# Performance work log

Measured on AMD Instinct MI355X. Metric: run time of the kernel, lower is better.

Reference implementation:

```python
import jax, jax.numpy as jnp
import numpy as np

K = 3  # hardcoded in TransitionUp.forward

def setup_inputs() -> dict:
    key = jax.random.key(0)
    ks = jax.random.split(key, 8)
    M, N = 32768, 8192
    UP_C, DOWN_C, OUT_C = 128, 256, 128
    return {
        "up_points": jax.random.normal(ks[0], (M, 3), dtype=jnp.float32),
        "up_features": jax.random.normal(ks[1], (M, UP_C), dtype=jnp.float32),
        "down_points": jax.random.normal(ks[2], (N, 3), dtype=jnp.float32),
        "down_features": jax.random.normal(ks[3], (N, DOWN_C), dtype=jnp.float32),
        # torch nn.Linear params: W [out,in], b [out]
        "W_up": jax.random.normal(ks[4], (OUT_C, UP_C), dtype=jnp.float32) / np.sqrt(UP_C),
        "b_up": jax.random.normal(ks[5], (OUT_C,), dtype=jnp.float32) * 0.01,
        "W_down": jax.random.normal(ks[6], (OUT_C, DOWN_C), dtype=jnp.float32) / np.sqrt(DOWN_C),
        "b_down": jax.random.normal(ks[7], (OUT_C,), dtype=jnp.float32) * 0.01,
    }

def interpolate_knn(query_points, dataset_points, dataset_features, k):
    # squared pairwise distances [M, N]
    delta = query_points[:, None, :] - dataset_points[None, :, :]
    dist = jnp.sum(delta * delta, axis=-1)
    neg_dist, knn_idx = jax.lax.top_k(-dist, k)  # smallest-k
    knn_dist = -neg_dist                           # [M, k]
    knn_feats = dataset_features[knn_idx]          # [M, k, C]
    recip = 1.0 / (knn_dist + 1e-8)
    weights = recip / jnp.sum(recip, axis=-1, keepdims=True)  # [M, k]
    return jnp.einsum('mk,mkc->mc', weights, knn_feats)

def reference(up_points, up_features, down_points, down_features, W_up, b_up, W_down, b_down):
    down_f = down_features @ W_down.T + b_down            # [N, OUT_C]
    interp_f = interpolate_knn(up_points, down_points, down_f, K)  # [M, OUT_C]
    return interp_f + (up_features @ W_up.T + b_up)
```

## Files before the change

kernel.cpp:

```cpp
#include <hip/hip_runtime.h>
#include <cfloat>

#define M_UP   32768
#define N_DOWN 8192
#define UPC    128
#define DOWNC  256
#define OUTC   128
#define NCHUNK 8
#define CHUNK  (N_DOWN / NCHUNK)
#define G      8
#define Q      2
#define PG     12

__device__ __forceinline__ void fma4(float4& acc, float s, const float4 w) {
    acc.x = fmaf(s, w.x, acc.x);
    acc.y = fmaf(s, w.y, acc.y);
    acc.z = fmaf(s, w.z, acc.z);
    acc.w = fmaf(s, w.w, acc.w);
}

__device__ __forceinline__ void top3_bl(float s, int idx,
                                        float& d0, float& d1, float& d2,
                                        int& i0, int& i1, int& i2) {
    bool c0 = s < d0, c1 = s < d1, c2 = s < d2;
    float n0 = fminf(d0, s);
    float n1 = __builtin_amdgcn_fmed3f(d0, d1, s);
    float n2 = __builtin_amdgcn_fmed3f(d1, d2, s);
    int m0 = c0 ? idx : i0;
    int m1 = c0 ? i0 : (c1 ? idx : i1);
    int m2 = c1 ? i1 : (c2 ? idx : i2);
    d0 = n0; d1 = n1; d2 = n2;
    i0 = m0; i1 = m1; i2 = m2;
}

__global__ __launch_bounds__(256) void transpose_w(
        const float* __restrict__ W_up, const float* __restrict__ W_down,
        float* __restrict__ wt_up, float* __restrict__ wt_down) {
    int e = blockIdx.x * 256 + threadIdx.x;
    if (e < DOWNC * OUTC) {
        int k = e >> 7, c = e & 127;
        wt_down[e] = W_down[c * DOWNC + k];
    } else {
        int e2 = e - DOWNC * OUTC;
        int k = e2 >> 7, c = e2 & 127;
        wt_up[e2] = W_up[c * UPC + k];
    }
}

template <int K>
__device__ __forceinline__ void gemm_tile32(
        const float* __restrict__ A, const float* __restrict__ WT,
        float* sA , float* sW ,
        int rbase, int tid, float4 acc[2][2]) {
    const int rl = tid & 15;
    const int c0 = (tid >> 4) * 8;
    #pragma unroll 1
    for (int ph = 0; ph < K / 32; ++ph) {
        if (ph) __syncthreads();
        {
            int r = tid >> 3, k4 = tid & 7;
            float4 v = *(const float4*)(A + (size_t)(rbase + r) * K + ph * 32 + k4 * 4);
            *(float4*)&sA[r * 36 + k4 * 4] = v;
        }
        #pragma unroll
        for (int i = 0; i < 4; ++i) {
            int idx = tid + i * 256;
            int kk = idx >> 5, cc = idx & 31;
            float4 v = *(const float4*)(WT + (size_t)(ph * 32 + kk) * OUTC + cc * 4);
            *(float4*)&sW[kk * OUTC + cc * 4] = v;
        }
        __syncthreads();
        #pragma unroll 4
        for (int kk = 0; kk < 32; ++kk) {
            float a0 = sA[rl * 36 + kk];
            float a1 = sA[(rl + 16) * 36 + kk];
            float4 w0 = *(const float4*)&sW[kk * OUTC + c0];
            float4 w1 = *(const float4*)&sW[kk * OUTC + c0 + 4];
            fma4(acc[0][0], a0, w0); fma4(acc[0][1], a0, w1);
            fma4(acc[1][0], a1, w0); fma4(acc[1][1], a1, w1);
        }
    }
}

__device__ __forceinline__ void down_body(
        const float* __restrict__ A, const float* __restrict__ WT,
        const float* __restrict__ bias, float* __restrict__ down_f,
        int rb, int tid, float* smem) {
    float* sA = smem;
    float* sW = smem + 1152;
    float4 acc[2][2] = {};
    gemm_tile32<DOWNC>(A, WT, sA, sW, rb * 32, tid, acc);
    const int rl = tid & 15;
    const int cg = (tid >> 4) * 2;
    const float4 b0 = ((const float4*)bias)[cg];
    const float4 b1 = ((const float4*)bias)[cg + 1];
    #pragma unroll
    for (int i = 0; i < 2; ++i) {
        const int row = rb * 32 + rl + 16 * i;
        float4 v0 = acc[i][0], v1 = acc[i][1];
        v0.x += b0.x; v0.y += b0.y; v0.z += b0.z; v0.w += b0.w;
        v1.x += b1.x; v1.y += b1.y; v1.z += b1.z; v1.w += b1.w;
        ((float4*)down_f)[row * 32 + cg] = v0;
        ((float4*)down_f)[row * 32 + cg + 1] = v1;
    }
}

__device__ __forceinline__ void knn_body(
        const float* __restrict__ up_points,
        const float* __restrict__ down_points,
        float2* __restrict__ part,
        int bx, int by, int tid, float* smem) {
    float* sx = smem;
    float* sy = smem + 1536;
    float* sz = smem + 3072;
    const int base = by * CHUNK;
    for (int t = tid; t < CHUNK; t += 256) {
        int g = base + t;
        int gi = t >> 3, j = t & 7;
        sx[PG * gi + j] = down_points[3 * g];
        sy[PG * gi + j] = down_points[3 * g + 1];
        sz[PG * gi + j] = down_points[3 * g + 2];
    }
    __syncthreads();

    const int m0 = bx * (256 * Q) + tid;
    const int m1 = m0 + 256;
    const float q0x = up_points[3 * m0];
    const float q0y = up_points[3 * m0 + 1];
    const float q0z = up_points[3 * m0 + 2];
    const float q1x = up_points[3 * m1];
    const float q1y = up_points[3 * m1 + 1];
    const float q1z = up_points[3 * m1 + 2];

    float a_gd0 = FLT_MAX, a_gd1 = FLT_MAX, a_gd2 = FLT_MAX;
    int   a_gi0 = 0, a_gi1 = 0, a_gi2 = 0;
    float b_gd0 = FLT_MAX, b_gd1 = FLT_MAX, b_gd2 = FLT_MAX;
    int   b_gi0 = 0, b_gi1 = 0, b_gi2 = 0;

    for (int gi = 0; gi < CHUNK / G; ++gi) {
        float4 x0 = *(const float4*)&sx[PG * gi], x1 = *(const float4*)&sx[PG * gi + 4];
        float4 y0 = *(const float4*)&sy[PG * gi], y1 = *(const float4*)&sy[PG * gi + 4];
        float4 z0 = *(const float4*)&sz[PG * gi], z1 = *(const float4*)&sz[PG * gi + 4];
        float px[G] = {x0.x, x0.y, x0.z, x0.w, x1.x, x1.y, x1.z, x1.w};
        float py[G] = {y0.x, y0.y, y0.z, y0.w, y1.x, y1.y, y1.z, y1.w};
        float pz[G] = {z0.x, z0.y, z0.z, z0.w, z1.x, z1.y, z1.z, z1.w};
        float s0[G], s1[G];
        #pragma unroll
        for (int j = 0; j < G; ++j) {
            float dx0 = q0x - px[j], dy0 = q0y - py[j], dz0 = q0z - pz[j];
            s0[j] = fmaf(dz0, dz0, fmaf(dy0, dy0, dx0 * dx0));
            float dx1 = q1x - px[j], dy1 = q1y - py[j], dz1 = q1z - pz[j];
            s1[j] = fmaf(dz1, dz1, fmaf(dy1, dy1, dx1 * dx1));
        }
        float gm0 = fminf(fminf(fminf(s0[0], s0[1]), fminf(s0[2], s0[3])),
                          fminf(fminf(s0[4], s0[5]), fminf(s0[6], s0[7])));
        float gm1 = fminf(fminf(fminf(s1[0], s1[1]), fminf(s1[2], s1[3])),
                          fminf(fminf(s1[4], s1[5]), fminf(s1[6], s1[7])));
        top3_bl(gm0, gi, a_gd0, a_gd1, a_gd2, a_gi0, a_gi1, a_gi2);
        top3_bl(gm1, gi, b_gd0, b_gd1, b_gd2, b_gi0, b_gi1, b_gi2);
    }

    #pragma unroll
    for (int qq = 0; qq < Q; ++qq) {
        const float qx = qq ? q1x : q0x;
        const float qy = qq ? q1y : q0y;
        const float qz = qq ? q1z : q0z;
        int bases[3];
        if (qq == 0) { bases[0] = a_gi0; bases[1] = a_gi1; bases[2] = a_gi2; }
        else         { bases[0] = b_gi0; bases[1] = b_gi1; bases[2] = b_gi2; }
        float D0 = FLT_MAX, D1 = FLT_MAX, D2 = FLT_MAX;
        int I0 = 0, I1 = 0, I2 = 0;
        #pragma unroll
        for (int t = 0; t < 3; ++t) {
            const int gb = bases[t];
            float4 x0 = *(const float4*)&sx[PG * gb], x1 = *(const float4*)&sx[PG * gb + 4];
            float4 y0 = *(const float4*)&sy[PG * gb], y1 = *(const float4*)&sy[PG * gb + 4];
            float4 z0 = *(const float4*)&sz[PG * gb], z1 = *(const float4*)&sz[PG * gb + 4];
            float px[G] = {x0.x, x0.y, x0.z, x0.w, x1.x, x1.y, x1.z, x1.w};
            float py[G] = {y0.x, y0.y, y0.z, y0.w, y1.x, y1.y, y1.z, y1.w};
            float pz[G] = {z0.x, z0.y, z0.z, z0.w, z1.x, z1.y, z1.z, z1.w};
            #pragma unroll
            for (int j = 0; j < G; ++j) {
                float dx = qx - px[j], dy = qy - py[j], dz = qz - pz[j];
                float s = fmaf(dz, dz, fmaf(dy, dy, dx * dx));
                top3_bl(s, base + gb * G + j, D0, D1, D2, I0, I1, I2);
            }
        }
        const int m = qq ? m1 : m0;
        const int o = (by * M_UP + m) * 3;
        part[o]     = make_float2(D0, __int_as_float(I0));
        part[o + 1] = make_float2(D1, __int_as_float(I1));
        part[o + 2] = make_float2(D2, __int_as_float(I2));
    }
}

__global__ __launch_bounds__(256) void fused_dp_knn(
        const float* __restrict__ down_features, const float* __restrict__ wt_down,
        const float* __restrict__ b_down, float* __restrict__ down_f,
        const float* __restrict__ up_points, const float* __restrict__ down_points,
        float2* __restrict__ part) {
    __shared__ __align__(16) float smem[5248];
    const int bid = blockIdx.x;
    if (bid < 512) {
        knn_body(up_points, down_points, part, bid & 63, bid >> 6,
                 threadIdx.x, smem);
    } else {
        down_body(down_features, wt_down, b_down, down_f, bid - 512,
                  threadIdx.x, smem);
    }
}

__global__ __launch_bounds__(256) void up_fused(
        const float* __restrict__ A, const float* __restrict__ WT,
        const float* __restrict__ bias, const float* __restrict__ down_f,
        const float2* __restrict__ part,
        float* __restrict__ out) {
    __shared__ __align__(16) float sAT[32][72];
    __shared__ __align__(16) float sW[32][128];
    const int tid = threadIdx.x;
    const int rt4 = (tid >> 4) * 4;
    const int ct  = tid & 15;
    const int rbase = blockIdx.x * 64;

    float4 acc[4][2] = {};
    #pragma unroll 1
    for (int ph = 0; ph < UPC / 32; ++ph) {
        if (ph) __syncthreads();
        {
            const int r = tid & 63, kq = tid >> 6;
            const float* Ar = A + (size_t)(rbase + r) * UPC + ph * 32 + kq * 8;
            float4 v0 = *(const float4*)Ar;
            float4 v1 = *(const float4*)(Ar + 4);
            const int k0 = kq * 8;
            sAT[k0 + 0][r] = v0.x; sAT[k0 + 1][r] = v0.y;
            sAT[k0 + 2][r] = v0.z; sAT[k0 + 3][r] = v0.w;
            sAT[k0 + 4][r] = v1.x; sAT[k0 + 5][r] = v1.y;
            sAT[k0 + 6][r] = v1.z; sAT[k0 + 7][r] = v1.w;
        }
        {
            const float4* Wp = (const float4*)(WT + (size_t)ph * 32 * OUTC);
            float4* sW4 = (float4*)&sW[0][0];
            #pragma unroll
            for (int i = 0; i < 4; ++i)
                sW4[tid + i * 256] = Wp[tid + i * 256];
        }
        __syncthreads();
        #pragma unroll 4
        for (int kk = 0; kk < 32; ++kk) {
            float4 a  = *(const float4*)&sAT[kk][rt4];
            float4 w0 = *(const float4*)&sW[kk][ct * 4];
            float4 w1 = *(const float4*)&sW[kk][64 + ct * 4];
            fma4(acc[0][0], a.x, w0); fma4(acc[0][1], a.x, w1);
            fma4(acc[1][0], a.y, w0); fma4(acc[1][1], a.y, w1);
            fma4(acc[2][0], a.z, w0); fma4(acc[2][1], a.z, w1);
            fma4(acc[3][0], a.w, w0); fma4(acc[3][1], a.w, w1);
        }
    }

    const float4 b0 = ((const float4*)bias)[ct];
    const float4 b1 = ((const float4*)bias)[ct + 16];
    const float4* df4 = (const float4*)down_f;
    float4* out4 = (float4*)out;
    #pragma unroll
    for (int i = 0; i < 4; ++i) {
        const int m = rbase + rt4 + i;
        float D0 = FLT_MAX, D1 = FLT_MAX, D2 = FLT_MAX;
        int I0 = 0, I1 = 0, I2 = 0;
        #pragma unroll
        for (int s = 0; s < NCHUNK; ++s) {
            const float2* p = part + ((size_t)s * M_UP + m) * 3;
            float2 v0 = p[0], v1 = p[1], v2 = p[2];
            top3_bl(v0.x, __float_as_int(v0.y), D0, D1, D2, I0, I1, I2);
            top3_bl(v1.x, __float_as_int(v1.y), D0, D1, D2, I0, I1, I2);
            top3_bl(v2.x, __float_as_int(v2.y), D0, D1, D2, I0, I1, I2);
        }
        float r0 = 1.f / (D0 + 1e-8f);
        float r1 = 1.f / (D1 + 1e-8f);
        float r2 = 1.f / (D2 + 1e-8f);
        float rs = (r0 + r1) + r2;
        float w0 = r0 / rs, w1 = r1 / rs, w2 = r2 / rs;
        float4 f00 = df4[I0 * 32 + ct], f01 = df4[I0 * 32 + ct + 16];
        float4 f10 = df4[I1 * 32 + ct], f11 = df4[I1 * 32 + ct + 16];
        float4 f20 = df4[I2 * 32 + ct], f21 = df4[I2 * 32 + ct + 16];
        float4 res0, res1;
        res0.x = acc[i][0].x + b0.x + fmaf(w0, f00.x, fmaf(w1, f10.x, w2 * f20.x));
        res0.y = acc[i][0].y + b0.y + fmaf(w0, f00.y, fmaf(w1, f10.y, w2 * f20.y));
        res0.z = acc[i][0].z + b0.z + fmaf(w0, f00.z, fmaf(w1, f10.z, w2 * f20.z));
        res0.w = acc[i][0].w + b0.w + fmaf(w0, f00.w, fmaf(w1, f10.w, w2 * f20.w));
        res1.x = acc[i][1].x + b1.x + fmaf(w0, f01.x, fmaf(w1, f11.x, w2 * f21.x));
        res1.y = acc[i][1].y + b1.y + fmaf(w0, f01.y, fmaf(w1, f11.y, w2 * f21.y));
        res1.z = acc[i][1].z + b1.z + fmaf(w0, f01.z, fmaf(w1, f11.z, w2 * f21.z));
        res1.w = acc[i][1].w + b1.w + fmaf(w0, f01.w, fmaf(w1, f11.w, w2 * f21.w));
        out4[m * 32 + ct] = res0;
        out4[m * 32 + ct + 16] = res1;
    }
}

extern "C" void kernel_launch(void* const* d_in, const int* in_sizes, int n_in,
                              void* d_out, int out_size, void* d_ws, size_t ws_size,
                              hipStream_t stream) {
    const float* up_points     = (const float*)d_in[0];
    const float* up_features   = (const float*)d_in[1];
    const float* down_points   = (const float*)d_in[2];
    const float* down_features = (const float*)d_in[3];
    const float* W_up          = (const float*)d_in[4];
    const float* b_up          = (const float*)d_in[5];
    const float* W_down        = (const float*)d_in[6];
    const float* b_down        = (const float*)d_in[7];
    float* out = (float*)d_out;

    float* wt_down = (float*)d_ws;
    float* wt_up   = wt_down + DOWNC * OUTC;
    float* down_f  = wt_up + UPC * OUTC;
    float2* part   = (float2*)(down_f + N_DOWN * OUTC);

    transpose_w<<<(DOWNC * OUTC + UPC * OUTC) / 256, 256, 0, stream>>>(
        W_up, W_down, wt_up, wt_down);
    fused_dp_knn<<<768, 256, 0, stream>>>(
        down_features, wt_down, b_down, down_f, up_points, down_points, part);
    up_fused<<<M_UP / 64, 256, 0, stream>>>(
        up_features, wt_up, b_up, down_f, part, out);
}
```

Before: 167.9 us.

## Move up-projection GEMM into fused kNN kernel and add separate merge pass

The up_features GEMM now runs as extra block roles inside the fused kNN/down-projection kernel, with block IDs interleaved 2 kNN : 1 down : 2 up per group of 5, so its work can overlap the compute-heavy kNN blocks. A new lightweight merge kernel stages the partial top-3 lists in shared memory, merges them, gathers down_f rows, and adds the interpolation into out with a read-modify-write. This trades an extra round trip of the output tensor through global memory and a larger shared allocation for better load balance across the GPU.

```diff
diff --git a/kernel.cpp b/kernel.cpp
--- a/kernel.cpp
+++ b/kernel.cpp
@@ -194,33 +194,15 @@
     }
 }
 
-__global__ __launch_bounds__(256) void fused_dp_knn(
-        const float* __restrict__ down_features, const float* __restrict__ wt_down,
-        const float* __restrict__ b_down, float* __restrict__ down_f,
-        const float* __restrict__ up_points, const float* __restrict__ down_points,
-        float2* __restrict__ part) {
-    __shared__ __align__(16) float smem[5248];
-    const int bid = blockIdx.x;
-    if (bid < 512) {
-        knn_body(up_points, down_points, part, bid & 63, bid >> 6,
-                 threadIdx.x, smem);
-    } else {
-        down_body(down_features, wt_down, b_down, down_f, bid - 512,
-                  threadIdx.x, smem);
-    }
-}
-
-__global__ __launch_bounds__(256) void up_fused(
+__device__ __forceinline__ void upg_body(
         const float* __restrict__ A, const float* __restrict__ WT,
-        const float* __restrict__ bias, const float* __restrict__ down_f,
-        const float2* __restrict__ part,
-        float* __restrict__ out) {
-    __shared__ __align__(16) float sAT[32][72];
-    __shared__ __align__(16) float sW[32][128];
-    const int tid = threadIdx.x;
+        const float* __restrict__ bias, float* __restrict__ out,
+        int rb, int tid, float* smem) {
+    float* sAT = smem;
+    float* sW  = smem + 2304;
     const int rt4 = (tid >> 4) * 4;
     const int ct  = tid & 15;
-    const int rbase = blockIdx.x * 64;
+    const int rbase = rb * 64;
 
     float4 acc[4][2] = {};
     #pragma unroll 1
@@ -232,14 +214,14 @@
             float4 v0 = *(const float4*)Ar;
             float4 v1 = *(const float4*)(Ar + 4);
             const int k0 = kq * 8;
-            sAT[k0 + 0][r] = v0.x; sAT[k0 + 1][r] = v0.y;
-            sAT[k0 + 2][r] = v0.z; sAT[k0 + 3][r] = v0.w;
-            sAT[k0 + 4][r] = v1.x; sAT[k0 + 5][r] = v1.y;
-            sAT[k0 + 6][r] = v1.z; sAT[k0 + 7][r] = v1.w;
+            sAT[(k0 + 0) * 72 + r] = v0.x; sAT[(k0 + 1) * 72 + r] = v0.y;
+            sAT[(k0 + 2) * 72 + r] = v0.z; sAT[(k0 + 3) * 72 + r] = v0.w;
+            sAT[(k0 + 4) * 72 + r] = v1.x; sAT[(k0 + 5) * 72 + r] = v1.y;
+            sAT[(k0 + 6) * 72 + r] = v1.z; sAT[(k0 + 7) * 72 + r] = v1.w;
         }
         {
             const float4* Wp = (const float4*)(WT + (size_t)ph * 32 * OUTC);
-            float4* sW4 = (float4*)&sW[0][0];
+            float4* sW4 = (float4*)sW;
             #pragma unroll
             for (int i = 0; i < 4; ++i)
                 sW4[tid + i * 256] = Wp[tid + i * 256];
@@ -247,29 +229,78 @@
         __syncthreads();
         #pragma unroll 4
         for (int kk = 0; kk < 32; ++kk) {
-            float4 a  = *(const float4*)&sAT[kk][rt4];
-            float4 w0 = *(const float4*)&sW[kk][ct * 4];
-            float4 w1 = *(const float4*)&sW[kk][64 + ct * 4];
+            float4 a  = *(const float4*)&sAT[kk * 72 + rt4];
+            float4 w0 = *(const float4*)&sW[kk * 128 + ct * 4];
+            float4 w1 = *(const float4*)&sW[kk * 128 + 64 + ct * 4];
             fma4(acc[0][0], a.x, w0); fma4(acc[0][1], a.x, w1);
             fma4(acc[1][0], a.y, w0); fma4(acc[1][1], a.y, w1);
             fma4(acc[2][0], a.z, w0); fma4(acc[2][1], a.z, w1);
             fma4(acc[3][0], a.w, w0); fma4(acc[3][1], a.w, w1);
         }
     }
-
     const float4 b0 = ((const float4*)bias)[ct];
     const float4 b1 = ((const float4*)bias)[ct + 16];
-    const float4* df4 = (const float4*)down_f;
     float4* out4 = (float4*)out;
     #pragma unroll
     for (int i = 0; i < 4; ++i) {
         const int m = rbase + rt4 + i;
+        float4 v0 = acc[i][0], v1 = acc[i][1];
+        v0.x += b0.x; v0.y += b0.y; v0.z += b0.z; v0.w += b0.w;
+        v1.x += b1.x; v1.y += b1.y; v1.z += b1.z; v1.w += b1.w;
+        out4[m * 32 + ct] = v0;
+        out4[m * 32 + ct + 16] = v1;
+    }
+}
+
+__global__ __launch_bounds__(256) void fused_dp_knn(
+        const float* __restrict__ down_features, const float* __restrict__ wt_down,
+        const float* __restrict__ b_down, float* __restrict__ down_f,
+        const float* __restrict__ up_points, const float* __restrict__ down_points,
+        float2* __restrict__ part,
+        const float* __restrict__ up_features, const float* __restrict__ wt_up,
+        const float* __restrict__ b_up, float* __restrict__ out) {
+    __shared__ __align__(16) float smem[6400];
+    const int bid = blockIdx.x;
+    const int grp = bid / 5, rid = bid % 5;
+    if (rid < 2) {
+        const int kidx = grp * 2 + rid;
+        knn_body(up_points, down_points, part, kidx & 63, kidx >> 6,
+                 threadIdx.x, smem);
+    } else if (rid == 2) {
+        down_body(down_features, wt_down, b_down, down_f, grp,
+                  threadIdx.x, smem);
+    } else {
+        const int uidx = grp * 2 + (rid - 3);
+        upg_body(up_features, wt_up, b_up, out, uidx, threadIdx.x, smem);
+    }
+}
+
+__global__ __launch_bounds__(256) void merge_out(
+        const float* __restrict__ down_f, const float2* __restrict__ part,
+        float* __restrict__ out) {
+    __shared__ __align__(16) float2 sPart[NCHUNK][48];
+    const int mb = blockIdx.x * 16;
+    for (int t = threadIdx.x; t < NCHUNK * 48; t += 256) {
+        int s = t / 48, j = t - s * 48;
+        sPart[s][j] = part[((size_t)s * M_UP + mb) * 3 + j];
+    }
+    __syncthreads();
+
+    const int c4 = threadIdx.x & 31;
+    const int rr = threadIdx.x >> 5;
+    const float4* df4 = (const float4*)down_f;
+    float4* out4 = (float4*)out;
+    #pragma unroll
+    for (int t = 0; t < 2; ++t) {
+        const int lr = rr + 8 * t;
+        const int m = mb + lr;
         float D0 = FLT_MAX, D1 = FLT_MAX, D2 = FLT_MAX;
         int I0 = 0, I1 = 0, I2 = 0;
         #pragma unroll
         for (int s = 0; s < NCHUNK; ++s) {
-            const float2* p = part + ((size_t)s * M_UP + m) * 3;
-            float2 v0 = p[0], v1 = p[1], v2 = p[2];
+            float2 v0 = sPart[s][lr * 3];
+            float2 v1 = sPart[s][lr * 3 + 1];
+            float2 v2 = sPart[s][lr * 3 + 2];
             top3_bl(v0.x, __float_as_int(v0.y), D0, D1, D2, I0, I1, I2);
             top3_bl(v1.x, __float_as_int(v1.y), D0, D1, D2, I0, I1, I2);
             top3_bl(v2.x, __float_as_int(v2.y), D0, D1, D2, I0, I1, I2);
@@ -279,20 +310,15 @@
         float r2 = 1.f / (D2 + 1e-8f);
         float rs = (r0 + r1) + r2;
         float w0 = r0 / rs, w1 = r1 / rs, w2 = r2 / rs;
-        float4 f00 = df4[I0 * 32 + ct], f01 = df4[I0 * 32 + ct + 16];
-        float4 f10 = df4[I1 * 32 + ct], f11 = df4[I1 * 32 + ct + 16];
-        float4 f20 = df4[I2 * 32 + ct], f21 = df4[I2 * 32 + ct + 16];
-        float4 res0, res1;
-        res0.x = acc[i][0].x + b0.x + fmaf(w0, f00.x, fmaf(w1, f10.x, w2 * f20.x));
-        res0.y = acc[i][0].y + b0.y + fmaf(w0, f00.y, fmaf(w1, f10.y, w2 * f20.y));
-        res0.z = acc[i][0].z + b0.z + fmaf(w0, f00.z, fmaf(w1, f10.z, w2 * f20.z));
-        res0.w = acc[i][0].w + b0.w + fmaf(w0, f00.w, fmaf(w1, f10.w, w2 * f20.w));
-        res1.x = acc[i][1].x + b1.x + fmaf(w0, f01.x, fmaf(w1, f11.x, w2 * f21.x));
-        res1.y = acc[i][1].y + b1.y + fmaf(w0, f01.y, fmaf(w1, f11.y, w2 * f21.y));
-        res1.z = acc[i][1].z + b1.z + fmaf(w0, f01.z, fmaf(w1, f11.z, w2 * f21.z));
-        res1.w = acc[i][1].w + b1.w + fmaf(w0, f01.w, fmaf(w1, f11.w, w2 * f21.w));
-        out4[m * 32 + ct] = res0;
-        out4[m * 32 + ct + 16] = res1;
+        float4 f0 = df4[I0 * 32 + c4];
+        float4 f1 = df4[I1 * 32 + c4];
+        float4 f2 = df4[I2 * 32 + c4];
+        float4 o = out4[m * 32 + c4];
+        o.x += fmaf(w0, f0.x, fmaf(w1, f1.x, w2 * f2.x));
+        o.y += fmaf(w0, f0.y, fmaf(w1, f1.y, w2 * f2.y));
+        o.z += fmaf(w0, f0.z, fmaf(w1, f1.z, w2 * f2.z));
+        o.w += fmaf(w0, f0.w, fmaf(w1, f1.w, w2 * f2.w));
+        out4[m * 32 + c4] = o;
     }
 }
 
@@ -316,8 +342,8 @@
 
     transpose_w<<<(DOWNC * OUTC + UPC * OUTC) / 256, 256, 0, stream>>>(
         W_up, W_down, wt_up, wt_down);
-    fused_dp_knn<<<768, 256, 0, stream>>>(
-        down_features, wt_down, b_down, down_f, up_points, down_points, part);
-    up_fused<<<M_UP / 64, 256, 0, stream>>>(
-        up_features, wt_up, b_up, down_f, part, out);
-}
+    fused_dp_knn<<<1280, 256, 0, stream>>>(
+        down_features, wt_down, b_down, down_f, up_points, down_points, part,
+        up_features, wt_up, b_up, out);
+    merge_out<<<M_UP / 16, 256, 0, stream>>>(down_f, part, out);
+}
```

After: 197.0 us. 1.17x slower.
